# Performance work log

Measured on AMD Instinct MI355X. Metric: run time of the kernel, lower is better.

## Reference

```python
import jax, jax.numpy as jnp
import numpy as np

B, T, E, H, V = 32, 256, 1024, 1024, 32000


def setup_inputs() -> dict:
    key = jax.random.key(0)
    ks = jax.random.split(key, 6)
    s = 0.02  # initrange-style scale
    return {
        "words": jax.random.randint(ks[0], (B, T), 0, V),
        "embed_w": jax.random.normal(ks[1], (V, E), dtype=jnp.float32) * s,
        "w_ih": jax.random.normal(ks[2], (4 * H, E), dtype=jnp.float32) * s,
        "w_hh": jax.random.normal(ks[3], (4 * H, H), dtype=jnp.float32) * s,
        "b_ih": jnp.zeros((4 * H,), jnp.float32),
        "b_hh": jnp.zeros((4 * H,), jnp.float32),
        "emit_w": jax.random.normal(ks[4], (V, H), dtype=jnp.float32) * s,
        "emit_b": jnp.zeros((V,), jnp.float32),
    }


def _lstm_cell(x, h, c, w_ih, w_hh, b_ih, b_hh):
    # PyTorch LSTMCell gate order: i, f, g, o
    gates = x @ w_ih.T + b_ih + h @ w_hh.T + b_hh  # [B, 4H]
    i, f, g, o = jnp.split(gates, 4, axis=-1)
    i = jax.nn.sigmoid(i)
    f = jax.nn.sigmoid(f)
    g = jnp.tanh(g)
    o = jax.nn.sigmoid(o)
    c_new = f * c + i * g
    h_new = o * jnp.tanh(c_new)
    return h_new, c_new


def reference(words, embed_w, w_ih, w_hh, b_ih, b_hh, emit_w, emit_b):
    emb = embed_w[words]  # [B, T, E]
    h0 = jnp.zeros((B, H), emb.dtype)
    c0 = jnp.zeros((B, H), emb.dtype)

    def step(carry, xs):
        h, c = carry
        x_t, w_t = xs  # x_t: [B,E], w_t: [B]
        h, c = _lstm_cell(x_t, h, c, w_ih, w_hh, b_ih, b_hh)
        logits = h @ emit_w.T + emit_b          # [B, V]
        logp = jax.nn.log_softmax(logits, -1)   # [B, V]
        ll = jnp.take_along_axis(logp, w_t[:, None], axis=1)[:, 0]  # [B]
        return (h, c), ll

    xs = (jnp.swapaxes(emb, 0, 1), jnp.swapaxes(words, 0, 1))  # time-major
    _, emit_ll = jax.lax.scan(step, (h0, c0), xs)
    return emit_ll  # [T, B] per-token log-likelihoods
```

## Files before the change

### kernel.cpp

```cpp
#include <hip/hip_runtime.h>
#include <stdint.h>

#define B_ 32
#define T_ 256
#define E_ 1024
#define H_ 1024
#define V_ 32000

typedef unsigned short u16;
typedef unsigned int   u32;
typedef unsigned long long u64;

typedef __attribute__((ext_vector_type(8))) short bf16x8;
typedef __attribute__((ext_vector_type(4))) float f32x4;

__device__ __forceinline__ float bf2f(u16 u){ u32 x = ((u32)u) << 16; return __uint_as_float(x); }
__device__ __forceinline__ u16  f2bf(float f){
  u32 x = __float_as_uint(f);
  u32 r = (x + 0x7fffu + ((x >> 16) & 1u)) >> 16;
  return (u16)r;
}
__device__ __forceinline__ float fsig(float x){ return 1.f / (1.f + __expf(-x)); }
__device__ __forceinline__ float ftanh(float x){
  float e = __expf(2.f * x);
  return 1.f - 2.f / (e + 1.f);
}

__device__ __forceinline__ void gload_lds16(const void* g, void* l){
  __builtin_amdgcn_global_load_lds((const __attribute__((address_space(1))) unsigned int*)g,
                                   (__attribute__((address_space(3))) unsigned int*)l, 16, 0, 0);
}

__global__ void k_prep_wc(const float* __restrict__ wih, const float* __restrict__ whh,
                          u16* __restrict__ Wc){
  int i = blockIdx.x * 256 + threadIdx.x;
  int r = i >> 9; int k4 = (i & 511) << 2;
  const float* src = (k4 < 1024) ? (wih + (size_t)r * 1024 + k4)
                                 : (whh + (size_t)r * 1024 + (k4 - 1024));
  float4 v = *(const float4*)src;
  u64 pk = (u64)f2bf(v.x) | ((u64)f2bf(v.y) << 16) | ((u64)f2bf(v.z) << 32) | ((u64)f2bf(v.w) << 48);
  *(u64*)(Wc + (size_t)r * 2048 + k4) = pk;
}

__global__ void k_prep_ew(const float* __restrict__ src, u16* __restrict__ dst){
  size_t i = (size_t)(blockIdx.x * 256 + threadIdx.x) * 4;
  float4 v = *(const float4*)(src + i);
  u64 pk = (u64)f2bf(v.x) | ((u64)f2bf(v.y) << 16) | ((u64)f2bf(v.z) << 32) | ((u64)f2bf(v.w) << 48);
  *(u64*)(dst + i) = pk;
}

__global__ void k_prep_bsum(const float* __restrict__ bih, const float* __restrict__ bhh,
                            float* __restrict__ bsum){
  int i = blockIdx.x * 256 + threadIdx.x;
  bsum[i] = bih[i] + bhh[i];
}

__global__ void k_gather_x(const int* __restrict__ words, const float* __restrict__ embed,
                           u16* __restrict__ X){
  int row = blockIdx.x;
  int t = row >> 5, b = row & 31;
  int wd = words[b * T_ + t];
  const float* src = embed + (size_t)wd * E_;
  u16* dst = X + (size_t)row * E_;
  int e = threadIdx.x * 4;
  float4 v = *(const float4*)(src + e);
  u64 pk = (u64)f2bf(v.x) | ((u64)f2bf(v.y) << 16) | ((u64)f2bf(v.z) << 32) | ((u64)f2bf(v.w) << 48);
  *(u64*)(dst + e) = pk;
}

__device__ __forceinline__ void stage_tile(const u16* __restrict__ Ab, const u16* __restrict__ Bb,
                                           int blog2, char* buf, int kk, int tid){
  char* As = buf;
  char* Bs = buf + 16384;
  int u0 = tid, r0 = u0 >> 2, s0 = (u0 & 3) ^ ((r0 >> 1) & 3);
  gload_lds16(Ab + (((size_t)r0) << 10) + kk * 32 + s0 * 8, As + (size_t)u0 * 16);
  int u1 = 512 + tid, r1 = u1 >> 2, s1 = (u1 & 3) ^ ((r1 >> 1) & 3);
  gload_lds16(Ab + (((size_t)r1) << 10) + kk * 32 + s1 * 8, As + (size_t)u1 * 16);
  int r2 = tid >> 2, s2 = (tid & 3) ^ ((r2 >> 1) & 3);
  gload_lds16(Bb + (((size_t)r2) << blog2) + kk * 32 + s2 * 8, Bs + (size_t)tid * 16);
}

__device__ __forceinline__ void tile_gemm(const u16* __restrict__ Ab, const u16* __restrict__ Bb,
                                          int blog2, char* sm, f32x4 (&acc)[4][4],
                                          int tid, int lane, int wr, int wc){
  stage_tile(Ab, Bb, blog2, sm, 0, tid);
  #pragma unroll 2
  for (int kk = 0; kk < 32; ++kk){
    char* cur = sm + (size_t)(kk & 1) * 24576;
    if (kk < 31){
      stage_tile(Ab, Bb, blog2, sm + (size_t)((kk + 1) & 1) * 24576, kk + 1, tid);
      asm volatile("s_waitcnt vmcnt(3)" ::: "memory");
    } else {
      asm volatile("s_waitcnt vmcnt(0)" ::: "memory");
    }
    __builtin_amdgcn_s_barrier();
    __builtin_amdgcn_sched_barrier(0);
    char* As = cur;
    char* Bs = cur + 16384;
    bf16x8 af[4], bfr[4];
    #pragma unroll
    for (int mi = 0; mi < 4; ++mi){
      int r = wr * 64 + mi * 16 + (lane & 15);
      u32 byte = ((u32)r << 6) + (((u32)lane >> 4) << 4);
      byte ^= (u32)(r & 6) << 3;
      af[mi] = *(const bf16x8*)(As + byte);
    }
    #pragma unroll
    for (int ni = 0; ni < 4; ++ni){
      int r = wc * 64 + ni * 16 + (lane & 15);
      u32 byte = ((u32)r << 6) + (((u32)lane >> 4) << 4);
      byte ^= (u32)(r & 6) << 3;
      bfr[ni] = *(const bf16x8*)(Bs + byte);
    }
    #pragma unroll
    for (int mi = 0; mi < 4; ++mi)
      #pragma unroll
      for (int ni = 0; ni < 4; ++ni)
        acc[mi][ni] = __builtin_amdgcn_mfma_f32_16x16x32_bf16(af[mi], bfr[ni], acc[mi][ni], 0, 0, 0);
    __builtin_amdgcn_s_barrier();
  }
}

__launch_bounds__(512, 2)
__global__ void k_xgemm(const u16* __restrict__ X, const u16* __restrict__ Wc,
                        const float* __restrict__ bsum, u16* __restrict__ Xg){
  __shared__ __align__(16) char smem[49152];
  const int tid = threadIdx.x, lane = tid & 63, w = tid >> 6;
  const int wr = w >> 1, wc = w & 1;
  const int mtx = blockIdx.x >> 5, vcx = blockIdx.x & 31;
  const u16* Ab = X + (size_t)mtx * 256 * 1024;
  const u16* Bb = Wc + (size_t)vcx * 128 * 2048;
  f32x4 acc[4][4];
  #pragma unroll
  for (int mi = 0; mi < 4; ++mi)
    #pragma unroll
    for (int ni = 0; ni < 4; ++ni){ f32x4 z = {0.f,0.f,0.f,0.f}; acc[mi][ni] = z; }
  tile_gemm(Ab, Bb, 11, smem, acc, tid, lane, wr, wc);
  float bcol[4];
  #pragma unroll
  for (int ni = 0; ni < 4; ++ni)
    bcol[ni] = bsum[vcx * 128 + wc * 64 + ni * 16 + (lane & 15)];
  int colb = vcx * 128 + wc * 64 + (lane & 15);
  int rowb = mtx * 256 + wr * 64 + ((lane >> 4) << 2);
  #pragma unroll
  for (int mi = 0; mi < 4; ++mi){
    #pragma unroll
    for (int ni = 0; ni < 4; ++ni){
      float b = bcol[ni];
      u32 lo = (u32)f2bf(acc[mi][ni][0] + b) | ((u32)f2bf(acc[mi][ni][1] + b) << 16);
      u32 hi = (u32)f2bf(acc[mi][ni][2] + b) | ((u32)f2bf(acc[mi][ni][3] + b) << 16);
      uint2 pk; pk.x = lo; pk.y = hi;
      *(uint2*)(Xg + (size_t)(colb + ni * 16) * 8192 + rowb + mi * 16) = pk;
    }
  }
}

__device__ __forceinline__ void emit_tile(u32 mt, u32 vc, const u16* __restrict__ Hall,
                                          const u16* __restrict__ Ew,
                                          const float* __restrict__ emit_b,
                                          float* __restrict__ parts,
                                          char* sm, int tid, int lane, int w){
  int wr = w >> 1, wc = w & 1;
  const u16* Ab = Hall + 32 * 1024 + (size_t)mt * 256 * 1024;
  const u16* Bb = Ew + (size_t)vc * 128 * 1024;
  f32x4 acc[4][4];
  #pragma unroll
  for (int mi = 0; mi < 4; ++mi)
    #pragma unroll
    for (int ni = 0; ni < 4; ++ni){ f32x4 z = {0.f,0.f,0.f,0.f}; acc[mi][ni] = z; }
  tile_gemm(Ab, Bb, 10, sm, acc, tid, lane, wr, wc);
  float* rs = (float*)(sm + 49152);
  float eb[4];
  #pragma unroll
  for (int ni = 0; ni < 4; ++ni)
    eb[ni] = emit_b[vc * 128 + wc * 64 + ni * 16 + (lane & 15)];
  #pragma unroll
  for (int mi = 0; mi < 4; ++mi){
    #pragma unroll
    for (int r = 0; r < 4; ++r){
      float s = 0.f;
      #pragma unroll
      for (int ni = 0; ni < 4; ++ni) s += __expf(acc[mi][ni][r] + eb[ni]);
      s += __shfl_xor(s, 1); s += __shfl_xor(s, 2); s += __shfl_xor(s, 4); s += __shfl_xor(s, 8);
      if ((lane & 15) == 0)
        rs[wc * 256 + wr * 64 + mi * 16 + ((lane >> 4) << 2) + r] = s;
    }
  }
  __syncthreads();
  if (tid < 256)
    parts[(size_t)vc * 8192 + (size_t)mt * 256 + tid] = rs[tid] + rs[256 + tid];
  __syncthreads();
}

__launch_bounds__(512, 2)
__global__ void k_mega(const u16* __restrict__ Wc, const u16* __restrict__ Xg,
                       const u16* __restrict__ Ew, const float* __restrict__ emit_b,
                       u16* __restrict__ Hall, float* __restrict__ parts,
                       u32* __restrict__ ctrl){
  __shared__ __align__(16) char smem[65536];
  u32* flags = ctrl + 1024;

  const int tid  = threadIdx.x;
  const int lane = tid & 63;
  const int w    = tid >> 6;
  const int bid  = blockIdx.x;

  if (bid >= 64){
    const int wid = bid - 64;
    for (u32 mt = 0; mt < 32; ++mt){
      if (w == 0){
        u32 tgtv = mt * 8u + 8u;
        u32 budget = 1u << 20;
        const u32* fp = flags + (lane << 5);
        for (;;){
          u32 fv;
          asm volatile("global_load_dword %0, %1, off sc0 sc1\n\ts_waitcnt vmcnt(0)"
                       : "=v"(fv) : "v"(fp) : "memory");
          if (__all((int)(fv >= tgtv)) || !--budget) break;
          __builtin_amdgcn_s_sleep(16);
        }
      }
      __syncthreads();
      for (u32 vc = (u32)wid; vc < 250u; vc += 192u)
        emit_tile(mt, vc, Hall, Ew, emit_b, parts, smem, tid, lane, w);
    }
    return;
  }

  const int nc0  = bid << 4;
  const int em   = tid >> 4, en = tid & 15;
  const int arow = lane & 15;
  const int akg  = (lane >> 4) << 3;
  float c = 0.f;
  float* Gp = (float*)smem;

  bf16x8 breg[4][4];
  {
    const u16* bp = Wc + (((size_t)(nc0 + arow)) << 11) + 1024 + (w << 7) + akg;
    #pragma unroll
    for (int g = 0; g < 4; ++g)
      #pragma unroll
      for (int kk = 0; kk < 4; ++kk)
        breg[g][kk] = *(const bf16x8*)(bp + (((size_t)g) << 21) + (kk << 5));
  }

  const u16* xgb = Xg + (size_t)(nc0 + en) * 8192 + em;

  for (int t = 0; t < T_; ++t){
    {
      const u32* fp = flags + ((8 * w + (lane & 7)) << 5);
      u32 budget = 1u << 22;
      u32 fv;
      do {
        asm volatile("global_load_dword %0, %1, off sc0 sc1\n\ts_waitcnt vmcnt(0)"
                     : "=v"(fv) : "v"(fp) : "memory");
      } while (!__all((int)(fv >= (u32)t)) && --budget);
    }
    uint4 a0[4], a1[4];
    {
      const u16* h0 = Hall + (((size_t)t) << 15) + (((size_t)arow) << 10) + (w << 7) + akg;
      const u16* h1 = h0 + 16384;
      #pragma unroll
      for (int kk = 0; kk < 4; ++kk){
        asm volatile("global_load_dwordx4 %0, %1, off offset:%2 sc0 sc1"
                     : "=v"(a0[kk]) : "v"(h0), "n"(kk * 64));
        asm volatile("global_load_dwordx4 %0, %1, off offset:%2 sc0 sc1"
                     : "=v"(a1[kk]) : "v"(h1), "n"(kk * 64));
      }
    }
    u16 x0 = xgb[(size_t)t * 32];
    u16 x1 = xgb[1024ull * 8192 + (size_t)t * 32];
    u16 x2 = xgb[2048ull * 8192 + (size_t)t * 32];
    u16 x3 = xgb[3072ull * 8192 + (size_t)t * 32];
    asm volatile("s_waitcnt vmcnt(0)" ::: "memory");
    __builtin_amdgcn_sched_barrier(0);

    f32x4 acc[4][2];
    #pragma unroll
    for (int g = 0; g < 4; ++g){ f32x4 z = {0.f,0.f,0.f,0.f}; acc[g][0] = z; acc[g][1] = z; }
    #pragma unroll
    for (int kk = 0; kk < 4; ++kk){
      bf16x8 f0 = __builtin_bit_cast(bf16x8, a0[kk]);
      bf16x8 f1 = __builtin_bit_cast(bf16x8, a1[kk]);
      #pragma unroll
      for (int g = 0; g < 4; ++g){
        acc[g][0] = __builtin_amdgcn_mfma_f32_16x16x32_bf16(f0, breg[g][kk], acc[g][0], 0, 0, 0);
        acc[g][1] = __builtin_amdgcn_mfma_f32_16x16x32_bf16(f1, breg[g][kk], acc[g][1], 0, 0, 0);
      }
    }
    #pragma unroll
    for (int g = 0; g < 4; ++g)
      #pragma unroll
      for (int mt2 = 0; mt2 < 2; ++mt2)
        #pragma unroll
        for (int r = 0; r < 4; ++r){
          int m = ((lane >> 4) << 2) + r + mt2 * 16;
          Gp[((w * 4 + g) * 32 + m) * 16 + (lane & 15)] = acc[g][mt2][r];
        }
    __syncthreads();

    {
      float s0 = bf2f(x0), s1 = bf2f(x1), s2 = bf2f(x2), s3 = bf2f(x3);
      #pragma unroll
      for (int p = 0; p < 8; ++p){
        s0 += Gp[((p * 4 + 0) * 32 + em) * 16 + en];
        s1 += Gp[((p * 4 + 1) * 32 + em) * 16 + en];
        s2 += Gp[((p * 4 + 2) * 32 + em) * 16 + en];
        s3 += Gp[((p * 4 + 3) * 32 + em) * 16 + en];
      }
      float ig = fsig(s0), fg = fsig(s1), gg = ftanh(s2), og = fsig(s3);
      c = fg * c + ig * gg;
      float h = og * ftanh(c);
      u32 hb = (u32)f2bf(h);
      const u16* hp = Hall + (((size_t)(t + 1)) << 15) + (((size_t)em) << 10) + nc0 + en;
      asm volatile("global_store_short %0, %1, off sc0 sc1" :: "v"(hp), "v"(hb) : "memory");
    }
    asm volatile("s_waitcnt vmcnt(0)" ::: "memory");
    __syncthreads();
    if (tid == 0){
      u32 fv = (u32)(t + 1);
      asm volatile("global_store_dword %0, %1, off sc0 sc1"
                   :: "v"(flags + (bid << 5)), "v"(fv) : "memory");
    }
  }
}

__global__ void k_target(const u16* __restrict__ Hall, const u16* __restrict__ Ew,
                         const int* __restrict__ words, const float* __restrict__ emit_b,
                         float* __restrict__ tgt){
  int row  = blockIdx.x * 4 + (threadIdx.x >> 6);
  int lane = threadIdx.x & 63;
  int t = row >> 5, b = row & 31;
  int wd = words[b * T_ + t];
  const bf16x8* ha = (const bf16x8*)(Hall + (size_t)(row + 32) * 1024 + lane * 16);
  const bf16x8* wa = (const bf16x8*)(Ew + (size_t)wd * 1024 + lane * 16);
  float s = 0.f;
  #pragma unroll
  for (int p = 0; p < 2; ++p){
    bf16x8 av = ha[p], wv = wa[p];
    #pragma unroll
    for (int i = 0; i < 8; ++i) s += bf2f((u16)av[i]) * bf2f((u16)wv[i]);
  }
  s += __shfl_xor(s, 32); s += __shfl_xor(s, 16); s += __shfl_xor(s, 8);
  s += __shfl_xor(s, 4);  s += __shfl_xor(s, 2);  s += __shfl_xor(s, 1);
  if (lane == 0) tgt[row] = s + emit_b[wd];
}

__global__ void k_final(const float* __restrict__ partials, const float* __restrict__ tgt,
                        float* __restrict__ out){
  int i = blockIdx.x * 256 + threadIdx.x;
  float s = 0.f;
  for (int vcb = 0; vcb < 250; ++vcb) s += partials[(size_t)vcb * 8192 + i];
  out[i] = tgt[i] - logf(s);
}

extern "C" void kernel_launch(void* const* d_in, const int* in_sizes, int n_in,
                              void* d_out, int out_size, void* d_ws, size_t ws_size,
                              hipStream_t stream){
  const int*   words = (const int*)d_in[0];
  const float* embed = (const float*)d_in[1];
  const float* wih   = (const float*)d_in[2];
  const float* whh   = (const float*)d_in[3];
  const float* bih   = (const float*)d_in[4];
  const float* bhh   = (const float*)d_in[5];
  const float* emw   = (const float*)d_in[6];
  const float* emb_b = (const float*)d_in[7];
  float* out = (float*)d_out;

  char* ws = (char*)d_ws;
  u16* Wc   = (u16*)ws;
  u16* Ew   = (u16*)(ws + 16777216);
  u16* X    = (u16*)(ws + 82313216);
  u16* Hall = (u16*)(ws + 99090432);
  u16* Xg   = (u16*)(ws + 115933184);
  float* bsum = (float*)(ws + 183042048);
  float* tgt  = (float*)(ws + 183058432);
  float* parts= (float*)(ws + 183091200);
  u32*  ctrl  = (u32*)(ws + 191283200);
  size_t need = 191283200ULL + 16384ULL;
  if (ws_size < need) return;

  hipMemsetAsync(ctrl, 0, 16384, stream);
  hipMemsetAsync(Hall, 0, 32 * 1024 * 2, stream);

  k_prep_wc  <<<8192,  256, 0, stream>>>(wih, whh, Wc);
  k_prep_ew  <<<32000, 256, 0, stream>>>(emw, Ew);
  k_prep_bsum<<<16,    256, 0, stream>>>(bih, bhh, bsum);
  k_gather_x <<<8192,  256, 0, stream>>>(words, embed, X);
  k_xgemm    <<<1024,  512, 0, stream>>>(X, Wc, bsum, Xg);
  k_mega     <<<256,   512, 0, stream>>>(Wc, Xg, Ew, emb_b, Hall, parts, ctrl);
  k_target   <<<2048,  256, 0, stream>>>(Hall, Ew, words, emb_b, tgt);
  k_final    <<<32,    256, 0, stream>>>(parts, tgt, out);
}
```

Baseline: 1.497 ms.

## Split fused LSTM/emit megakernel into separate recurrence and emit GEMM kernels

Removes the flag-polling emit blocks from the persistent LSTM kernel and runs the emit logsumexp-partial GEMM as a separate full-grid kernel after the recurrence finishes. This eliminates spin-wait polling and contention for CUs, L2 and HBM bandwidth during the latency-critical recurrence, and gives the emit GEMM the whole GPU. In exchange it loses the overlap of emit work with the serial recurrence, so the emit GEMM time is added to the critical path.

```diff
diff --git a/kernel.cpp b/kernel.cpp
--- a/kernel.cpp
+++ b/kernel.cpp
@@ -155,48 +155,9 @@
   }
 }
 
-__device__ __forceinline__ void emit_tile(u32 mt, u32 vc, const u16* __restrict__ Hall,
-                                          const u16* __restrict__ Ew,
-                                          const float* __restrict__ emit_b,
-                                          float* __restrict__ parts,
-                                          char* sm, int tid, int lane, int w){
-  int wr = w >> 1, wc = w & 1;
-  const u16* Ab = Hall + 32 * 1024 + (size_t)mt * 256 * 1024;
-  const u16* Bb = Ew + (size_t)vc * 128 * 1024;
-  f32x4 acc[4][4];
-  #pragma unroll
-  for (int mi = 0; mi < 4; ++mi)
-    #pragma unroll
-    for (int ni = 0; ni < 4; ++ni){ f32x4 z = {0.f,0.f,0.f,0.f}; acc[mi][ni] = z; }
-  tile_gemm(Ab, Bb, 10, sm, acc, tid, lane, wr, wc);
-  float* rs = (float*)(sm + 49152);
-  float eb[4];
-  #pragma unroll
-  for (int ni = 0; ni < 4; ++ni)
-    eb[ni] = emit_b[vc * 128 + wc * 64 + ni * 16 + (lane & 15)];
-  #pragma unroll
-  for (int mi = 0; mi < 4; ++mi){
-    #pragma unroll
-    for (int r = 0; r < 4; ++r){
-      float s = 0.f;
-      #pragma unroll
-      for (int ni = 0; ni < 4; ++ni) s += __expf(acc[mi][ni][r] + eb[ni]);
-      s += __shfl_xor(s, 1); s += __shfl_xor(s, 2); s += __shfl_xor(s, 4); s += __shfl_xor(s, 8);
-      if ((lane & 15) == 0)
-        rs[wc * 256 + wr * 64 + mi * 16 + ((lane >> 4) << 2) + r] = s;
-    }
-  }
-  __syncthreads();
-  if (tid < 256)
-    parts[(size_t)vc * 8192 + (size_t)mt * 256 + tid] = rs[tid] + rs[256 + tid];
-  __syncthreads();
-}
-
 __launch_bounds__(512, 2)
-__global__ void k_mega(const u16* __restrict__ Wc, const u16* __restrict__ Xg,
-                       const u16* __restrict__ Ew, const float* __restrict__ emit_b,
-                       u16* __restrict__ Hall, float* __restrict__ parts,
-                       u32* __restrict__ ctrl){
+__global__ void k_lstm(const u16* __restrict__ Wc, const u16* __restrict__ Xg,
+                       u16* __restrict__ Hall, u32* __restrict__ ctrl){
   __shared__ __align__(16) char smem[65536];
   u32* flags = ctrl + 1024;
 
@@ -204,28 +165,6 @@
   const int lane = tid & 63;
   const int w    = tid >> 6;
   const int bid  = blockIdx.x;
-
-  if (bid >= 64){
-    const int wid = bid - 64;
-    for (u32 mt = 0; mt < 32; ++mt){
-      if (w == 0){
-        u32 tgtv = mt * 8u + 8u;
-        u32 budget = 1u << 20;
-        const u32* fp = flags + (lane << 5);
-        for (;;){
-          u32 fv;
-          asm volatile("global_load_dword %0, %1, off sc0 sc1\n\ts_waitcnt vmcnt(0)"
-                       : "=v"(fv) : "v"(fp) : "memory");
-          if (__all((int)(fv >= tgtv)) || !--budget) break;
-          __builtin_amdgcn_s_sleep(16);
-        }
-      }
-      __syncthreads();
-      for (u32 vc = (u32)wid; vc < 250u; vc += 192u)
-        emit_tile(mt, vc, Hall, Ew, emit_b, parts, smem, tid, lane, w);
-    }
-    return;
-  }
 
   const int nc0  = bid << 4;
   const int em   = tid >> 4, en = tid & 15;
@@ -325,6 +264,44 @@
   }
 }
 
+__launch_bounds__(512, 2)
+__global__ void k_emit(const u16* __restrict__ Hall, const u16* __restrict__ Ew,
+                       const float* __restrict__ emit_b, float* __restrict__ parts){
+  __shared__ __align__(16) char smem[51200];
+  const int tid = threadIdx.x, lane = tid & 63, w = tid >> 6;
+  const int wr = w >> 1, wc = w & 1;
+  const u32 vc = blockIdx.x;
+  const u32 mt = blockIdx.y;
+  const u16* Ab = Hall + 32 * 1024 + (size_t)mt * 256 * 1024;
+  const u16* Bb = Ew + (size_t)vc * 128 * 1024;
+  f32x4 acc[4][4];
+  #pragma unroll
+  for (int mi = 0; mi < 4; ++mi)
+    #pragma unroll
+    for (int ni = 0; ni < 4; ++ni){ f32x4 z = {0.f,0.f,0.f,0.f}; acc[mi][ni] = z; }
+  tile_gemm(Ab, Bb, 10, smem, acc, tid, lane, wr, wc);
+  float* rs = (float*)(smem + 49152);
+  float eb[4];
+  #pragma unroll
+  for (int ni = 0; ni < 4; ++ni)
+    eb[ni] = emit_b[vc * 128 + wc * 64 + ni * 16 + (lane & 15)];
+  #pragma unroll
+  for (int mi = 0; mi < 4; ++mi){
+    #pragma unroll
+    for (int r = 0; r < 4; ++r){
+      float s = 0.f;
+      #pragma unroll
+      for (int ni = 0; ni < 4; ++ni) s += __expf(acc[mi][ni][r] + eb[ni]);
+      s += __shfl_xor(s, 1); s += __shfl_xor(s, 2); s += __shfl_xor(s, 4); s += __shfl_xor(s, 8);
+      if ((lane & 15) == 0)
+        rs[wc * 256 + wr * 64 + mi * 16 + ((lane >> 4) << 2) + r] = s;
+    }
+  }
+  __syncthreads();
+  if (tid < 256)
+    parts[(size_t)vc * 8192 + (size_t)mt * 256 + tid] = rs[tid] + rs[256 + tid];
+}
+
 __global__ void k_target(const u16* __restrict__ Hall, const u16* __restrict__ Ew,
                          const int* __restrict__ words, const float* __restrict__ emit_b,
                          float* __restrict__ tgt){
@@ -388,7 +365,8 @@
   k_prep_bsum<<<16,    256, 0, stream>>>(bih, bhh, bsum);
   k_gather_x <<<8192,  256, 0, stream>>>(words, embed, X);
   k_xgemm    <<<1024,  512, 0, stream>>>(X, Wc, bsum, Xg);
-  k_mega     <<<256,   512, 0, stream>>>(Wc, Xg, Ew, emb_b, Hall, parts, ctrl);
+  k_lstm     <<<64,    512, 0, stream>>>(Wc, Xg, Hall, ctrl);
+  k_emit     <<<dim3(250, 32), 512, 0, stream>>>(Hall, Ew, emb_b, parts);
   k_target   <<<2048,  256, 0, stream>>>(Hall, Ew, words, emb_b, tgt);
   k_final    <<<32,    256, 0, stream>>>(parts, tgt, out);
 }
```

Result: slower. 1.950 ms (+30.3%).
